# Kernel tuning notes

Measured on AMD Instinct MI355X. Metric: run time of the kernel, lower is better.

## Reference

```python
import jax, jax.numpy as jnp
import numpy as np

BLOCK = 64
THRESH = 0.95
EPS = 1e-8


def setup_inputs() -> dict:
    key = jax.random.key(0)
    kq, kk, kv = jax.random.split(key, 3)
    S, D = 4096, 128
    q = jax.random.normal(kq, (S, D), dtype=jnp.float32)
    k = jax.random.normal(kk, (S, D), dtype=jnp.float32)
    v = jax.random.normal(kv, (S, D), dtype=jnp.float32)
    return {"q": q, "k": k, "v": v}


def reference(q, k, v):
    S, D = q.shape
    nb = S // BLOCK
    qb = q.reshape(nb, BLOCK, D)
    kb = k.reshape(nb, BLOCK, D)
    vb = v.reshape(nb, BLOCK, D)
    # all block-pair scores: [nb_q, nb_k, BLOCK_q, BLOCK_k]
    scores = jnp.einsum('ibd,jcd->ijbc', qb, kb)
    m = jnp.max(scores, axis=-1, keepdims=True)
    e = jnp.exp(scores - m)
    s = jnp.sum(e, axis=-1, keepdims=True)  # per-block-pair softmax denominator
    # top-p truncation mask: sort descending, cumsum, threshold
    srt = jnp.sort(e, axis=-1)[..., ::-1]
    cum = jnp.cumsum(srt, axis=-1)
    mask = cum < THRESH * s
    # NOTE: faithful to original — mask (in sorted order) is applied to the
    # UNSORTED exp_scores, exactly as the torch code does (indices unused).
    em = e * mask
    em = em / (jnp.sum(em, axis=-1, keepdims=True) + EPS)
    # accumulate over key blocks j (per-pair normalized weights, summed)
    out = jnp.einsum('ijbc,jcd->ibd', em, vb)
    return out.reshape(S, D)
```

## Files before the change

### kernel.cpp

```cpp
#include <hip/hip_runtime.h>
#include <cstdint>
#include <cstddef>


#define SEQ   4096
#define DIM   128
#define BLK   64
#define NB    (SEQ / BLK)
#define NJG   16
#define JPB   (NB / NJG)
#define NT    256
#define PSTR  12288
#define THRESH 0.95f
#define EPSF   1e-8f

typedef __attribute__((ext_vector_type(8))) _Float16 f16x8;
typedef __attribute__((ext_vector_type(4))) float    f32x4;

#define MFMAH(a, b, c) __builtin_amdgcn_mfma_f32_16x16x32_f16((a), (b), (c), 0, 0, 0)

union UH4 { uint2 u; _Float16 h[4]; };
union UH8 { uint4 u; f16x8 v; };

__device__ __forceinline__ void gll16(const uint* g, uint* l) {
  __builtin_amdgcn_global_load_lds(
      (const __attribute__((address_space(1))) void*)g,
      (__attribute__((address_space(3))) void*)l, 16, 0, 0);
}

__global__ __launch_bounds__(NT, 4) void eco_prep_kernel(
    const float* __restrict__ K, const float* __restrict__ V,
    uint* __restrict__ P, float* __restrict__ O) {
  const int tid  = threadIdx.x;
  const int b    = blockIdx.x;
  const int jb   = b >> 2;
  const int part = b & 3;

  {
    float4 z = {0.f, 0.f, 0.f, 0.f};
    float4* op = (float4*)O;
#pragma unroll
    for (int it = 0; it < 2; ++it) op[b * 512 + it * NT + tid] = z;
  }

  {
    const float4* gk = (const float4*)(K + (size_t)jb * BLK * DIM);
    uint* dst = P + (size_t)jb * PSTR;
#pragma unroll
    for (int it = 0; it < 2; ++it) {
      int f = part * 512 + it * NT + tid;
      int r = f >> 5, c4 = f & 31;
      float4 x = gk[f];
      float xs[4] = {x.x, x.y, x.z, x.w};
      UH4 uh, ur;
#pragma unroll
      for (int e = 0; e < 4; ++e) {
        float v = xs[e];
        _Float16 h = (_Float16)v;
        uh.h[e] = h;
        ur.h[e] = (_Float16)(v - (float)h);
      }
      uint off = (uint)r * 64u + (((uint)(c4 >> 1) ^ (uint)(r & 15)) << 2) +
                 (uint)((c4 & 1) << 1);
      *(uint2*)&dst[off]        = uh.u;
      *(uint2*)&dst[4096 + off] = ur.u;
    }
  }

  {
    const float* gv = V + (size_t)jb * BLK * DIM;
    uint4* dv = (uint4*)(P + (size_t)jb * PSTR + 8192);
    int idx = part * 256 + tid;
    int ch = idx >> 7, d = idx & 127;
    UH8 u;
#pragma unroll
    for (int j = 0; j < 8; ++j)
      u.v[j] = (_Float16)gv[(ch * 8 + j) * DIM + d];
    dv[idx] = u.u;
  }
}

#define CE(x, y, dmax) { float _hi = fmaxf((x), (y)); float _lo = fminf((x), (y)); \
                         (x) = (dmax) ? _hi : _lo; (y) = (dmax) ? _lo : _hi; }

__global__ __launch_bounds__(NT, 4) void eco_attn_kernel(
    const float* __restrict__ Q, const uint* __restrict__ P,
    float* __restrict__ O) {
  __shared__ __align__(16) uint sK[8192];
  __shared__ __align__(16) uint sW[2048];

  const int tid  = threadIdx.x;
  const int ib   = blockIdx.y;
  const int jg   = blockIdx.x;
  const int lane = tid & 63;
  const int wv   = tid >> 6;
  const int quad = lane >> 4;
  const int l16  = lane & 15;
  const int q4   = quad << 2;

  uint* sWw = sW + wv * 512;

  f16x8 qh[4], qr[4];
  {
    const float* qp = Q + (size_t)(ib * BLK + wv * 16 + l16) * DIM + quad * 8;
#pragma unroll
    for (int ks = 0; ks < 4; ++ks) {
      float4 x0 = *(const float4*)(qp + ks * 32);
      float4 x1 = *(const float4*)(qp + ks * 32 + 4);
      float xs[8] = {x0.x, x0.y, x0.z, x0.w, x1.x, x1.y, x1.z, x1.w};
      f16x8 h8, r8;
#pragma unroll
      for (int e = 0; e < 8; ++e) {
        float v = xs[e];
        _Float16 h = (_Float16)v;
        h8[e] = h;
        r8[e] = (_Float16)(v - (float)h);
      }
      qh[ks] = h8; qr[ks] = r8;
    }
  }

  const f32x4 zf = {0.f, 0.f, 0.f, 0.f};
  f32x4 pv[8];
#pragma unroll
  for (int i = 0; i < 8; ++i) pv[i] = zf;

  {
    const uint* gsrc = P + (size_t)(jg * JPB) * PSTR;
#pragma unroll
    for (int it = 0; it < 8; ++it) {
      int idx = (it * NT + tid) << 2;
      gll16(gsrc + idx, sK + idx);
    }
  }

  for (int jj = 0; jj < JPB; ++jj) {
    const int jb = jg * JPB + jj;
    __syncthreads();

    f32x4 ah[4], ar[4];
#pragma unroll
    for (int nt = 0; nt < 4; ++nt) { ah[nt] = zf; ar[nt] = zf; }
#pragma unroll
    for (int nt = 0; nt < 4; ++nt) {
      const int rB = nt * 16 + l16;
      const uint rowoff = (uint)rB * 64u;
      const uint swk = (uint)(rB & 15);
#pragma unroll
      for (int ks = 0; ks < 4; ++ks) {
        uint off = rowoff + ((((uint)(ks * 4 + quad)) ^ swk) << 2);
        f16x8 bh = *(const f16x8*)&sK[off];
        f16x8 br = *(const f16x8*)&sK[4096 + off];
        ah[nt] = MFMAH(bh, qh[ks], ah[nt]);
        ar[nt] = MFMAH(br, qh[ks], ar[nt]);
        ar[nt] = MFMAH(bh, qr[ks], ar[nt]);
      }
    }
    __syncthreads();

    if (jj + 1 < JPB) {
      const uint* gsrc = P + (size_t)(jb + 1) * PSTR;
#pragma unroll
      for (int it = 0; it < 8; ++it) {
        int idx = (it * NT + tid) << 2;
        gll16(gsrc + idx, sK + idx);
      }
    }

    {
      float a[16], e[16];
#pragma unroll
      for (int nt = 0; nt < 4; ++nt) {
        f32x4 s = ah[nt] + ar[nt];
#pragma unroll
        for (int rg = 0; rg < 4; ++rg) a[nt * 4 + rg] = s[rg];
      }
      float mt[8];
#pragma unroll
      for (int i = 0; i < 8; ++i) mt[i] = fmaxf(a[i], a[i + 8]);
#pragma unroll
      for (int w2 = 4; w2 >= 1; w2 >>= 1)
#pragma unroll
        for (int i = 0; i < w2; ++i) mt[i] = fmaxf(mt[i], mt[i + w2]);
      float m = mt[0];
      m = fmaxf(m, __shfl_xor(m, 16, 64));
      m = fmaxf(m, __shfl_xor(m, 32, 64));
#pragma unroll
      for (int i = 0; i < 16; ++i) { a[i] = __expf(a[i] - m); e[i] = a[i]; }
      float st[8];
#pragma unroll
      for (int i = 0; i < 8; ++i) st[i] = a[i] + a[i + 8];
#pragma unroll
      for (int w2 = 4; w2 >= 1; w2 >>= 1)
#pragma unroll
        for (int i = 0; i < w2; ++i) st[i] += st[i + w2];
      float sr = st[0];
      sr += __shfl_xor(sr, 16, 64);
      sr += __shfl_xor(sr, 32, 64);
      const float T = THRESH * sr;

      const int s = quad;
#pragma unroll
      for (int k2 = 2; k2 <= 8; k2 <<= 1)
#pragma unroll
        for (int j2 = k2 >> 1; j2 >= 1; j2 >>= 1)
#pragma unroll
          for (int i = 0; i < 16; ++i) {
            int l = i ^ j2;
            if (l > i) { bool d = ((i & k2) == 0); CE(a[i], a[l], d); }
          }
      const bool x16 = ((s & 1) == 0);
      const bool x32 = ((s & 2) == 0);
#pragma unroll
      for (int j2 = 8; j2 >= 1; j2 >>= 1)
#pragma unroll
        for (int i = 0; i < 16; ++i) {
          int l = i ^ j2;
          if (l > i) { CE(a[i], a[l], x16); }
        }
      {
        const bool km = (x32 == x16);
#pragma unroll
        for (int i = 0; i < 16; ++i) {
          float o = __shfl_xor(a[i], 16, 64);
          a[i] = km ? fmaxf(a[i], o) : fminf(a[i], o);
        }
#pragma unroll
        for (int j2 = 8; j2 >= 1; j2 >>= 1)
#pragma unroll
          for (int i = 0; i < 16; ++i) {
            int l = i ^ j2;
            if (l > i) { CE(a[i], a[l], x32); }
          }
      }
      {
#pragma unroll
        for (int i = 0; i < 16; ++i) {
          float o = __shfl_xor(a[i], 32, 64);
          a[i] = x32 ? fmaxf(a[i], o) : fminf(a[i], o);
        }
#pragma unroll
        for (int i = 0; i < 16; ++i) {
          float o = __shfl_xor(a[i], 16, 64);
          a[i] = x16 ? fmaxf(a[i], o) : fminf(a[i], o);
        }
#pragma unroll
        for (int j2 = 8; j2 >= 1; j2 >>= 1)
#pragma unroll
          for (int i = 0; i < 16; ++i) {
            int l = i ^ j2;
            if (l > i) { CE(a[i], a[l], true); }
          }
      }
#pragma unroll
      for (int i = 1; i < 16; ++i) a[i] += a[i - 1];
      float tot = a[15];
      float c = tot;
      float o1 = __shfl_up(c, 16, 64); if (s >= 1) c += o1;
      float o2 = __shfl_up(c, 32, 64); if (s >= 2) c += o2;
      const float excl = c - tot;
      int cnt = 0;
#pragma unroll
      for (int i = 0; i < 16; ++i) cnt += ((a[i] + excl) < T) ? 1 : 0;
      cnt += __shfl_xor(cnt, 16, 64);
      cnt += __shfl_xor(cnt, 32, 64);
      const int t = cnt;
      float p = 0.f;
#pragma unroll
      for (int i = 0; i < 16; ++i) {
        int kidx = ((i >> 2) << 4) + q4 + (i & 3);
        p += (kidx < t) ? e[i] : 0.f;
      }
      p += __shfl_xor(p, 16, 64);
      p += __shfl_xor(p, 32, 64);
      const float rn = 1.0f / (p + EPSF);
      uint* wrow = sWw + l16 * 32;
#pragma unroll
      for (int nt = 0; nt < 4; ++nt) {
        UH4 u;
#pragma unroll
        for (int rg = 0; rg < 4; ++rg) {
          int kidx = nt * 16 + q4 + rg;
          float w = (kidx < t) ? e[nt * 4 + rg] * rn : 0.f;
          u.h[rg] = (_Float16)w;
        }
        uint c4 = (uint)(nt * 4 + quad);
        *(uint2*)&wrow[(c4 ^ (uint)l16) << 1] = u.u;
      }
    }
    __builtin_amdgcn_wave_barrier();

    f16x8 wf[2];
#pragma unroll
    for (int ks2 = 0; ks2 < 2; ++ks2) {
      uint c0 = (uint)(ks2 * 8 + quad * 2);
      const uint* wrow = sWw + l16 * 32;
      uint2 lo = *(const uint2*)&wrow[(c0 ^ (uint)l16) << 1];
      uint2 hi = *(const uint2*)&wrow[((c0 + 1) ^ (uint)l16) << 1];
      UH8 u;
      u.u = make_uint4(lo.x, lo.y, hi.x, hi.y);
      wf[ks2] = u.v;
    }
    {
      const uint* gvt = P + (size_t)jb * PSTR + 8192;
#pragma unroll
      for (int nt2 = 0; nt2 < 8; ++nt2) {
#pragma unroll
        for (int ks2 = 0; ks2 < 2; ++ks2) {
          f16x8 vf = *(const f16x8*)&gvt[((uint)((ks2 * 4 + quad) * 128 +
                                                 nt2 * 16 + l16)) << 2];
          pv[nt2] = MFMAH(wf[ks2], vf, pv[nt2]);
        }
      }
    }
  }

#pragma unroll
  for (int nt2 = 0; nt2 < 8; ++nt2) {
    const int col  = nt2 * 16 + l16;
    const int row0 = ib * BLK + wv * 16 + quad * 4;
#pragma unroll
    for (int rg = 0; rg < 4; ++rg)
      atomicAdd(O + (size_t)(row0 + rg) * DIM + col, pv[nt2][rg]);
  }
}

extern "C" void kernel_launch(void* const* d_in, const int* in_sizes, int n_in,
                              void* d_out, int out_size, void* d_ws, size_t ws_size,
                              hipStream_t stream) {
  (void)in_sizes; (void)n_in; (void)ws_size; (void)out_size;
  const float* q = (const float*)d_in[0];
  const float* k = (const float*)d_in[1];
  const float* v = (const float*)d_in[2];
  float* out = (float*)d_out;
  uint* prep = (uint*)d_ws;

  eco_prep_kernel<<<dim3(NB * 4), dim3(NT), 0, stream>>>(k, v, prep, out);
  eco_attn_kernel<<<dim3(NJG, NB), dim3(NT), 0, stream>>>(q, prep, out);
}
```

Before: 119.0 us.

## Permute K rows to keep softmax weights in registers and rebalance j-groups

K rows are permuted during the pack step so that the QK^T MFMA output layout already matches the A-operand layout needed for the PV MFMA. The probability weights can then be built directly in registers, which removes the per-wave LDS scratch (sW), its stores, the wave barrier and the reloads. The key-block split is also changed from 16 groups of 4 to 20 uneven groups (4 groups of 4 and 16 of 3), and launch bounds are raised to 5 waves per SIMD. The uneven grouping adds load imbalance, and a fifth workgroup may not fit because of register pressure or the host grid dimension.

```diff
diff --git a/kernel.cpp b/kernel.cpp
--- a/kernel.cpp
+++ b/kernel.cpp
@@ -7,8 +7,7 @@
 #define DIM   128
 #define BLK   64
 #define NB    (SEQ / BLK)
-#define NJG   16
-#define JPB   (NB / NJG)
+#define NJG   20
 #define NT    256
 #define PSTR  12288
 #define THRESH 0.95f
@@ -50,7 +49,9 @@
     for (int it = 0; it < 2; ++it) {
       int f = part * 512 + it * NT + tid;
       int r = f >> 5, c4 = f & 31;
-      float4 x = gk[f];
+      int nt = r >> 4, q = (r >> 2) & 3, rg = r & 3;
+      int o  = (nt & 1) * 32 + q * 8 + ((nt >> 1) << 2) + rg;
+      float4 x = gk[o * 32 + c4];
       float xs[4] = {x.x, x.y, x.z, x.w};
       UH4 uh, ur;
 #pragma unroll
@@ -83,11 +84,10 @@
 #define CE(x, y, dmax) { float _hi = fmaxf((x), (y)); float _lo = fminf((x), (y)); \
                          (x) = (dmax) ? _hi : _lo; (y) = (dmax) ? _lo : _hi; }
 
-__global__ __launch_bounds__(NT, 4) void eco_attn_kernel(
+__global__ __launch_bounds__(NT, 5) void eco_attn_kernel(
     const float* __restrict__ Q, const uint* __restrict__ P,
     float* __restrict__ O) {
   __shared__ __align__(16) uint sK[8192];
-  __shared__ __align__(16) uint sW[2048];
 
   const int tid  = threadIdx.x;
   const int ib   = blockIdx.y;
@@ -96,9 +96,10 @@
   const int wv   = tid >> 6;
   const int quad = lane >> 4;
   const int l16  = lane & 15;
-  const int q4   = quad << 2;
-
-  uint* sWw = sW + wv * 512;
+  const int q8   = quad << 3;
+
+  const int jb0 = (jg < 4) ? (4 * jg) : (16 + 3 * (jg - 4));
+  const int nj  = (jg < 4) ? 4 : 3;
 
   f16x8 qh[4], qr[4];
   {
@@ -126,7 +127,7 @@
   for (int i = 0; i < 8; ++i) pv[i] = zf;
 
   {
-    const uint* gsrc = P + (size_t)(jg * JPB) * PSTR;
+    const uint* gsrc = P + (size_t)jb0 * PSTR;
 #pragma unroll
     for (int it = 0; it < 8; ++it) {
       int idx = (it * NT + tid) << 2;
@@ -134,8 +135,9 @@
     }
   }
 
-  for (int jj = 0; jj < JPB; ++jj) {
-    const int jb = jg * JPB + jj;
+  for (int jj = 0; jj < nj; ++jj) {
+    const int jb = jb0 + jj;
+    const uint* gvt = P + (size_t)jb * PSTR + 8192;
     __syncthreads();
 
     f32x4 ah[4], ar[4];
@@ -158,7 +160,7 @@
     }
     __syncthreads();
 
-    if (jj + 1 < JPB) {
+    if (jj + 1 < nj) {
       const uint* gsrc = P + (size_t)(jb + 1) * PSTR;
 #pragma unroll
       for (int it = 0; it < 8; ++it) {
@@ -167,6 +169,7 @@
       }
     }
 
+    f16x8 wf[2];
     {
       float a[16], e[16];
 #pragma unroll
@@ -268,49 +271,35 @@
       float p = 0.f;
 #pragma unroll
       for (int i = 0; i < 16; ++i) {
-        int kidx = ((i >> 2) << 4) + q4 + (i & 3);
+        int nt = i >> 2, rg = i & 3;
+        int kidx = ((nt & 1) << 5) + q8 + ((nt >> 1) << 2) + rg;
         p += (kidx < t) ? e[i] : 0.f;
       }
       p += __shfl_xor(p, 16, 64);
       p += __shfl_xor(p, 32, 64);
       const float rn = 1.0f / (p + EPSF);
-      uint* wrow = sWw + l16 * 32;
-#pragma unroll
-      for (int nt = 0; nt < 4; ++nt) {
-        UH4 u;
-#pragma unroll
-        for (int rg = 0; rg < 4; ++rg) {
-          int kidx = nt * 16 + q4 + rg;
-          float w = (kidx < t) ? e[nt * 4 + rg] * rn : 0.f;
-          u.h[rg] = (_Float16)w;
-        }
-        uint c4 = (uint)(nt * 4 + quad);
-        *(uint2*)&wrow[(c4 ^ (uint)l16) << 1] = u.u;
-      }
-    }
-    __builtin_amdgcn_wave_barrier();
-
-    f16x8 wf[2];
-#pragma unroll
-    for (int ks2 = 0; ks2 < 2; ++ks2) {
-      uint c0 = (uint)(ks2 * 8 + quad * 2);
-      const uint* wrow = sWw + l16 * 32;
-      uint2 lo = *(const uint2*)&wrow[(c0 ^ (uint)l16) << 1];
-      uint2 hi = *(const uint2*)&wrow[((c0 + 1) ^ (uint)l16) << 1];
-      UH8 u;
-      u.u = make_uint4(lo.x, lo.y, hi.x, hi.y);
-      wf[ks2] = u.v;
-    }
-    {
-      const uint* gvt = P + (size_t)jb * PSTR + 8192;
-#pragma unroll
-      for (int nt2 = 0; nt2 < 8; ++nt2) {
-#pragma unroll
-        for (int ks2 = 0; ks2 < 2; ++ks2) {
-          f16x8 vf = *(const f16x8*)&gvt[((uint)((ks2 * 4 + quad) * 128 +
-                                                 nt2 * 16 + l16)) << 2];
-          pv[nt2] = MFMAH(wf[ks2], vf, pv[nt2]);
-        }
+#pragma unroll
+      for (int ks2 = 0; ks2 < 2; ++ks2) {
+        UH8 u;
+#pragma unroll
+        for (int jhi = 0; jhi < 2; ++jhi)
+#pragma unroll
+          for (int rg = 0; rg < 4; ++rg) {
+            int kidx = (ks2 << 5) + q8 + (jhi << 2) + rg;
+            float w = (kidx < t) ? e[(2 * jhi + ks2) * 4 + rg] * rn : 0.f;
+            u.v[jhi * 4 + rg] = (_Float16)w;
+          }
+        wf[ks2] = u.v;
+      }
+    }
+
+#pragma unroll
+    for (int nt2 = 0; nt2 < 8; ++nt2) {
+#pragma unroll
+      for (int ks2 = 0; ks2 < 2; ++ks2) {
+        f16x8 vf = *(const f16x8*)&gvt[((uint)((ks2 * 4 + quad) * 128 +
+                                               nt2 * 16 + l16)) << 2];
+        pv[nt2] = MFMAH(wf[ks2], vf, pv[nt2]);
       }
     }
   }
```

After: 157.0 us. +32.0%, slower.
